# Kernel optimization log

Measured on AMD Instinct MI355X. Metric: run time of the kernel, lower is better.

## Reference

```python
import jax, jax.numpy as jnp
import numpy as np

N = 30000   # nodes
E = 240000  # edges
G = 16      # graphs in batch
DIMS = [1, 256, 512, 1024]
OUT = 1024

def _xavier(key, fan_in, fan_out):
    lim = float(np.sqrt(6.0 / (fan_in + fan_out)))
    return jax.random.uniform(key, (fan_in, fan_out), minval=-lim, maxval=lim, dtype=jnp.float32)

def setup_inputs() -> dict:
    key = jax.random.key(0)
    ks = jax.random.split(key, 8)
    x = jax.random.normal(ks[0], (N, DIMS[0]), dtype=jnp.float32)
    edge_index = jax.random.randint(ks[1], (2, E), 0, N, dtype=jnp.int64)
    batch = jnp.sort(jax.random.randint(ks[2], (N,), 0, G, dtype=jnp.int64))
    W1 = _xavier(ks[3], DIMS[0], DIMS[1]); b1 = jnp.zeros((DIMS[1],), jnp.float32)
    W2 = _xavier(ks[4], DIMS[1], DIMS[2]); b2 = jnp.zeros((DIMS[2],), jnp.float32)
    W3 = _xavier(ks[5], DIMS[2], DIMS[3]); b3 = jnp.zeros((DIMS[3],), jnp.float32)
    Wo = _xavier(ks[6], DIMS[3], OUT);     bo = jnp.zeros((OUT,), jnp.float32)
    return {"x": x, "edge_index": edge_index, "batch": batch,
            "W1": W1, "b1": b1, "W2": W2, "b2": b2, "W3": W3, "b3": b3,
            "Wo": Wo, "bo": bo}

def reference(x, edge_index, batch, W1, b1, W2, b2, W3, b3, Wo, bo):
    n = x.shape[0]
    loops = jnp.arange(n)
    # GCNConv adds self-loops, then symmetric deg^-1/2 normalization
    src = jnp.concatenate([edge_index[0], loops])
    dst = jnp.concatenate([edge_index[1], loops])
    deg = jnp.zeros((n,), jnp.float32).at[dst].add(1.0)  # >=1 due to self-loops
    dis = jax.lax.rsqrt(deg)
    norm = (dis[src] * dis[dst])[:, None]  # [E+N, 1]

    def gcn(h, W, b):
        h = h @ W                                   # linear (no bias in lin)
        agg = jnp.zeros_like(h).at[dst].add(h[src] * norm)  # scatter-add messages
        return agg + b                              # GCNConv bias

    h = jax.nn.relu(gcn(x, W1, b1))
    h = jax.nn.relu(gcn(h, W2, b2))
    h = jax.nn.relu(gcn(h, W3, b3))
    # global mean pool over graphs
    sums = jnp.zeros((G, h.shape[1]), h.dtype).at[batch].add(h)
    cnt = jnp.zeros((G,), h.dtype).at[batch].add(1.0)
    pooled = sums / jnp.maximum(cnt, 1.0)[:, None]
    return pooled @ Wo + bo
```

## Files before the change

### kernel.cpp

```cpp
#include <hip/hip_runtime.h>
#include <hip/hip_bf16.h>
#include <stdint.h>

#define N_NODES 30000
#define E_EDGES 240000
#define NGRAPH  16
#define D1      256
#define D2      512
#define D3      1024
#define DOUT    1024
#define M_PAD   30720
#define NT_M    240
#define CAP     40

typedef unsigned short ushort_t;
typedef short short8 __attribute__((ext_vector_type(8)));
typedef float f32x4 __attribute__((ext_vector_type(4)));

__device__ __forceinline__ float bf2f(ushort_t u) {
    union { unsigned int i; float f; } v; v.i = ((unsigned int)u) << 16; return v.f;
}
__device__ __forceinline__ ushort_t f2bf(float x) {
    union { float f; unsigned int i; } v; v.f = x;
    unsigned int r = v.i + 0x7fffu + ((v.i >> 16) & 1u);
    return (ushort_t)(r >> 16);
}

__device__ __forceinline__ void gl_lds16(const ushort_t* g, ushort_t* l) {
    __builtin_amdgcn_global_load_lds(
        (const __attribute__((address_space(1))) void*)(g),
        (__attribute__((address_space(3))) void*)(l), 16, 0, 0);
}

__global__ void k_detect(const void* w1, const void* ei, int* flags) {
    int lane = threadIdx.x & 63;
    const ushort_t* h = (const ushort_t*)w1;
    float v = fabsf(bf2f(h[lane * 2]));
    unsigned long long badf = __ballot(!(v <= 0.25f));
    const int* e = (const int*)ei;
    unsigned long long badi = __ballot(e[lane * 2 + 1] != 0);
    if (threadIdx.x == 0) {
        flags[0] = (badf == 0ull) ? 1 : 0;
        flags[1] = (badi == 0ull) ? 1 : 0;
    }
}

__global__ void k_setup(const void* x, const void* batch, const void* w1, const void* b1,
                        const void* b2, const void* b3, const void* bo,
                        const void* W2, const void* W3,
                        float* xf, int* batch32, float* W1f, float* b1f, float* b2f,
                        float* b3f, float* bof, ushort_t* Wt2, ushort_t* Wt3,
                        int* slotcnt, float* pooled, float* pooled2, const int* flags) {
    int isbf = flags[0];
    int bid = blockIdx.x;
    int tid = threadIdx.x;
    if (bid < 492) {
        int i = bid * 256 + tid;
        if (i < 3072) {
            const void* src; float* dst; int idx;
            if      (i < 256)  { src = w1; dst = W1f; idx = i; }
            else if (i < 512)  { src = b1; dst = b1f; idx = i - 256; }
            else if (i < 1024) { src = b2; dst = b2f; idx = i - 512; }
            else if (i < 2048) { src = b3; dst = b3f; idx = i - 1024; }
            else               { src = bo; dst = bof; idx = i - 2048; }
            dst[idx] = isbf ? bf2f(((const ushort_t*)src)[idx]) : ((const float*)src)[idx];
        } else if (i < 33072) {
            int idx = i - 3072;
            xf[idx] = isbf ? bf2f(((const ushort_t*)x)[idx]) : ((const float*)x)[idx];
        } else if (i < 63072) {
            int idx = i - 33072;
            batch32[idx] = flags[1] ? (int)((const long long*)batch)[idx]
                                    : ((const int*)batch)[idx];
        } else if (i < 93072) {
            slotcnt[i - 63072] = 0;
        } else if (i < 109456) {
            pooled[i - 93072] = 0.0f;
        } else if (i < 125840) {
            pooled2[i - 109456] = 0.0f;
        }
    } else {
        __shared__ ushort_t tile[32][33];
        int tb = bid - 492;
        const void* in; ushort_t* out; int R, C, bx, by;
        if (tb < 128) { in = W2; out = Wt2; R = D1; C = D2; bx = tb & 15; by = tb >> 4; }
        else { tb -= 128; in = W3; out = Wt3; R = D2; C = D3; bx = tb & 31; by = tb >> 5; }
        int tx = tid & 31, ty = tid >> 5;
        int c0 = bx * 32, r0 = by * 32;
        for (int i = ty; i < 32; i += 8) {
            size_t idx = (size_t)(r0 + i) * C + c0 + tx;
            tile[i][tx] = isbf ? ((const ushort_t*)in)[idx] : f2bf(((const float*)in)[idx]);
        }
        __syncthreads();
        for (int i = ty; i < 32; i += 8) out[(size_t)(c0 + i) * R + r0 + tx] = tile[tx][i];
    }
}

__global__ void k_edge_count(const void* ei, int* slotcnt, int* slots, const int* flags) {
    int e = blockIdx.x * 256 + threadIdx.x;
    if (e >= E_EDGES) return;
    int s, d;
    if (flags[1]) {
        s = (int)((const long long*)ei)[e];
        d = (int)((const long long*)ei)[E_EDGES + e];
    } else {
        s = ((const int*)ei)[e];
        d = ((const int*)ei)[E_EDGES + e];
    }
    if ((unsigned)s >= N_NODES || (unsigned)d >= N_NODES) return;
    int pos = atomicAdd(&slotcnt[d], 1);
    if (pos < CAP) slots[d * CAP + pos] = s;
}

__global__ void k_s1(const float* xf, const int* slotcnt, const int* slots,
                     const int* batch, float* dis, float* s1, float* cntg) {
    int b = blockIdx.x;
    if (b == 118) {
        int g = threadIdx.x;
        if (g >= NGRAPH) return;
        int lo0 = 0, hi0 = N_NODES;
        while (lo0 < hi0) { int m = (lo0 + hi0) >> 1; if (batch[m] < g) lo0 = m + 1; else hi0 = m; }
        int lo1 = lo0, hi1 = N_NODES;
        while (lo1 < hi1) { int m = (lo1 + hi1) >> 1; if (batch[m] < g + 1) lo1 = m + 1; else hi1 = m; }
        cntg[g] = (float)(lo1 - lo0);
        return;
    }
    int d = b * 256 + threadIdx.x;
    if (d >= N_NODES) return;
    int cd = slotcnt[d];
    float di = rsqrtf(1.0f + (float)cd);
    dis[d] = di;
    int cnt = cd < CAP ? cd : CAP;
    float acc = xf[d] * di;
    for (int k = 0; k < cnt; k++) {
        int s = slots[d * CAP + k];
        acc += xf[s] * rsqrtf(1.0f + (float)slotcnt[s]);
    }
    s1[d] = acc * di;
}

__global__ void k_agg1(const float* s1, const float* W1f, const float* b1f,
                       ushort_t* a2, const int* slots, const int* slotcnt, const float* dis) {
    int node = blockIdx.x * 4 + (threadIdx.x >> 6);
    int lane = threadIdx.x & 63;
    int c4 = lane * 4;
    float w[4], bb[4], a[4];
    #pragma unroll
    for (int j = 0; j < 4; j++) { w[j] = W1f[c4 + j]; bb[j] = b1f[c4 + j]; }
    float di = dis[node];
    int cnt = slotcnt[node]; cnt = cnt < CAP ? cnt : CAP;
    float sv = s1[node];
    float wsl = di * di;
    #pragma unroll
    for (int j = 0; j < 4; j++) a[j] = wsl * fmaxf(sv * w[j] + bb[j], 0.0f);
    for (int k = 0; k < cnt; k++) {
        int s = slots[node * CAP + k];
        float ss = s1[s];
        float wn = dis[s] * di;
        #pragma unroll
        for (int j = 0; j < 4; j++) a[j] += wn * fmaxf(ss * w[j] + bb[j], 0.0f);
    }
    uint2 o;
    o.x = (unsigned int)f2bf(a[0]) | ((unsigned int)f2bf(a[1]) << 16);
    o.y = (unsigned int)f2bf(a[2]) | ((unsigned int)f2bf(a[3]) << 16);
    *(uint2*)&a2[(size_t)node * D1 + c4] = o;
}

__global__ void k_agg2(const ushort_t* h, ushort_t* out, const int* slots,
                       const int* slotcnt, const float* dis) {
    int node = blockIdx.x * 4 + (threadIdx.x >> 6);
    int lane = threadIdx.x & 63;
    int c8 = lane * 8;
    float di = dis[node];
    int cnt = slotcnt[node]; cnt = cnt < CAP ? cnt : CAP;
    float w = di * di;
    const ushort_t* hp = h + c8;
    short8 p = *(const short8*)&hp[(size_t)node * D2];
    float a[8];
    #pragma unroll
    for (int j = 0; j < 8; j++) a[j] = w * bf2f((ushort_t)p[j]);
    if (cnt > 0) {
        int s0 = slots[node * CAP];
        short8 q0 = *(const short8*)&hp[(size_t)s0 * D2];
        float ws0 = dis[s0] * di;
        for (int k = 1; k < cnt; k++) {
            int s1i = slots[node * CAP + k];
            short8 q1 = *(const short8*)&hp[(size_t)s1i * D2];
            float ws1 = dis[s1i] * di;
            #pragma unroll
            for (int j = 0; j < 8; j++) a[j] += ws0 * bf2f((ushort_t)q0[j]);
            q0 = q1; ws0 = ws1;
        }
        #pragma unroll
        for (int j = 0; j < 8; j++) a[j] += ws0 * bf2f((ushort_t)q0[j]);
    }
    uint4 o;
    o.x = (unsigned int)f2bf(a[0]) | ((unsigned int)f2bf(a[1]) << 16);
    o.y = (unsigned int)f2bf(a[2]) | ((unsigned int)f2bf(a[3]) << 16);
    o.z = (unsigned int)f2bf(a[4]) | ((unsigned int)f2bf(a[5]) << 16);
    o.w = (unsigned int)f2bf(a[6]) | ((unsigned int)f2bf(a[7]) << 16);
    *(uint4*)&out[(size_t)node * D2 + c8] = o;
}

__global__ __launch_bounds__(256, 4) void k_gemm(const ushort_t* A, const ushort_t* Bt,
                                                 const float* bias, ushort_t* Cmat,
                                                 int K, int Ncols, int ntn) {
    __shared__ __align__(16) ushort_t As[2][128 * 32];
    __shared__ __align__(16) ushort_t Bs[2][128 * 32];
    int tid = threadIdx.x;
    int id = blockIdx.x;
    int xcd = id & 7, q = id >> 3;
    int rt = xcd * (NT_M / 8) + q / ntn;
    int ct = q % ntn;
    int bm0 = rt * 128, bn0 = ct * 128;
    int wave = tid >> 6, lane = tid & 63;
    int wm = (wave & 1) * 64, wn = (wave >> 1) * 64;
    int l15 = lane & 15, quad = lane >> 4;

    int m1 = tid >> 2, k1 = (tid & 3) << 3;
    int off1 = m1 * 32 + k1, off2 = off1 + 64 * 32;
    const ushort_t* pA1 = A + (size_t)(bm0 + m1) * K + k1;
    const ushort_t* pA2 = pA1 + (size_t)64 * K;
    const ushort_t* pB1 = Bt + (size_t)(bn0 + m1) * K + k1;
    const ushort_t* pB2 = pB1 + (size_t)64 * K;

    gl_lds16(pA1, &As[0][off1]); gl_lds16(pA2, &As[0][off2]);
    gl_lds16(pB1, &Bs[0][off1]); gl_lds16(pB2, &Bs[0][off2]);

    f32x4 acc[4][4];
    for (int a = 0; a < 4; a++)
        for (int b = 0; b < 4; b++)
            acc[a][b] = (f32x4){0.f, 0.f, 0.f, 0.f};

    int niter = K >> 5;
    for (int it = 0; it < niter; ++it) {
        __syncthreads();
        int cb = it & 1;
        int ktn = (it + 1) << 5;
        if (ktn < K) {
            int wb = cb ^ 1;
            gl_lds16(pA1 + ktn, &As[wb][off1]); gl_lds16(pA2 + ktn, &As[wb][off2]);
            gl_lds16(pB1 + ktn, &Bs[wb][off1]); gl_lds16(pB2 + ktn, &Bs[wb][off2]);
        }
        short8 af[4], bfr[4];
        for (int im = 0; im < 4; im++)
            af[im] = *(const short8*)&As[cb][(wm + im * 16 + l15) * 32 + quad * 8];
        for (int in = 0; in < 4; in++)
            bfr[in] = *(const short8*)&Bs[cb][(wn + in * 16 + l15) * 32 + quad * 8];
        for (int im = 0; im < 4; im++)
            for (int in = 0; in < 4; in++)
                acc[im][in] = __builtin_amdgcn_mfma_f32_16x16x32_bf16(af[im], bfr[in], acc[im][in], 0, 0, 0);
    }

    for (int im = 0; im < 4; im++) {
        int row = bm0 + wm + im * 16 + quad * 4;
        for (int in = 0; in < 4; in++) {
            int col = bn0 + wn + in * 16 + l15;
            float bv = bias[col];
            for (int r = 0; r < 4; r++) {
                float v = acc[im][in][r] + bv;
                v = v > 0.0f ? v : 0.0f;
                Cmat[(size_t)(row + r) * Ncols + col] = f2bf(v);
            }
        }
    }
}

__global__ __launch_bounds__(256, 4) void k_gemm_pool(const ushort_t* A, const ushort_t* Bt,
                                                      const float* bias, const int* batch,
                                                      float* pooled, int K, int ntn) {
    __shared__ __align__(16) ushort_t As[2][128 * 32];
    __shared__ __align__(16) ushort_t Bs[2][128 * 32];
    int tid = threadIdx.x;
    int id = blockIdx.x;
    int xcd = id & 7, q = id >> 3;
    int rt = xcd * (NT_M / 8) + q / ntn;
    int ct = q % ntn;
    int bm0 = rt * 128, bn0 = ct * 128;
    int wave = tid >> 6, lane = tid & 63;
    int wm = (wave & 1) * 64, wn = (wave >> 1) * 64;
    int l15 = lane & 15, quad = lane >> 4;

    int m1 = tid >> 2, k1 = (tid & 3) << 3;
    int off1 = m1 * 32 + k1, off2 = off1 + 64 * 32;
    const ushort_t* pA1 = A + (size_t)(bm0 + m1) * K + k1;
    const ushort_t* pA2 = pA1 + (size_t)64 * K;
    const ushort_t* pB1 = Bt + (size_t)(bn0 + m1) * K + k1;
    const ushort_t* pB2 = pB1 + (size_t)64 * K;

    gl_lds16(pA1, &As[0][off1]); gl_lds16(pA2, &As[0][off2]);
    gl_lds16(pB1, &Bs[0][off1]); gl_lds16(pB2, &Bs[0][off2]);

    f32x4 acc[4][4];
    for (int a = 0; a < 4; a++)
        for (int b = 0; b < 4; b++)
            acc[a][b] = (f32x4){0.f, 0.f, 0.f, 0.f};

    int niter = K >> 5;
    for (int it = 0; it < niter; ++it) {
        __syncthreads();
        int cb = it & 1;
        int ktn = (it + 1) << 5;
        if (ktn < K) {
            int wb = cb ^ 1;
            gl_lds16(pA1 + ktn, &As[wb][off1]); gl_lds16(pA2 + ktn, &As[wb][off2]);
            gl_lds16(pB1 + ktn, &Bs[wb][off1]); gl_lds16(pB2 + ktn, &Bs[wb][off2]);
        }
        short8 af[4], bfr[4];
        for (int im = 0; im < 4; im++)
            af[im] = *(const short8*)&As[cb][(wm + im * 16 + l15) * 32 + quad * 8];
        for (int in = 0; in < 4; in++)
            bfr[in] = *(const short8*)&Bs[cb][(wn + in * 16 + l15) * 32 + quad * 8];
        for (int im = 0; im < 4; im++)
            for (int in = 0; in < 4; in++)
                acc[im][in] = __builtin_amdgcn_mfma_f32_16x16x32_bf16(af[im], bfr[in], acc[im][in], 0, 0, 0);
    }

    __syncthreads();
    float* pl = (float*)&As[0][0];
    int* gtile = (int*)&Bs[0][0];
    for (int i = tid; i < NGRAPH * 128; i += 256) pl[i] = 0.0f;
    if (tid < 128) {
        int r = bm0 + tid; if (r > N_NODES - 1) r = N_NODES - 1;
        int g = batch[r]; g = g < 0 ? 0 : (g > NGRAPH - 1 ? NGRAPH - 1 : g);
        gtile[tid] = g;
    }
    __syncthreads();

    int gmin = gtile[0], gmax = gtile[127];
    if (gmin == gmax && bm0 + 127 < N_NODES) {
        float csum[4];
        #pragma unroll
        for (int in = 0; in < 4; in++) csum[in] = 0.0f;
        for (int im = 0; im < 4; im++) {
            #pragma unroll
            for (int in = 0; in < 4; in++) {
                float bv = bias[bn0 + wn + in * 16 + l15];
                #pragma unroll
                for (int r = 0; r < 4; r++)
                    csum[in] += fmaxf(acc[im][in][r] + bv, 0.0f);
            }
        }
        #pragma unroll
        for (int in = 0; in < 4; in++) {
            csum[in] += __shfl_xor(csum[in], 16);
            csum[in] += __shfl_xor(csum[in], 32);
        }
        if (quad == 0) {
            #pragma unroll
            for (int in = 0; in < 4; in++)
                atomicAdd(&pl[gmin * 128 + wn + in * 16 + l15], csum[in]);
        }
    } else {
        for (int im = 0; im < 4; im++) {
            int rl = wm + im * 16 + quad * 4;
            for (int in = 0; in < 4; in++) {
                int cl = wn + in * 16 + l15;
                float bv = bias[bn0 + cl];
                float vsum = 0.0f;
                int gprev = gtile[rl];
                for (int r = 0; r < 4; r++) {
                    int row = bm0 + rl + r;
                    float v = (row < N_NODES) ? fmaxf(acc[im][in][r] + bv, 0.0f) : 0.0f;
                    int g = gtile[rl + r];
                    if (g != gprev) {
                        atomicAdd(&pl[gprev * 128 + cl], vsum);
                        vsum = 0.0f; gprev = g;
                    }
                    vsum += v;
                }
                atomicAdd(&pl[gprev * 128 + cl], vsum);
            }
        }
    }
    __syncthreads();

    int span = (gmax - gmin + 1) * 128;
    for (int idx = tid; idx < span; idx += 256) {
        int g = gmin + (idx >> 7), cl = idx & 127;
        float v = pl[g * 128 + cl];
        if (v != 0.0f) atomicAdd(&pooled[g * DOUT + bn0 + cl], v);
    }
}

__global__ __launch_bounds__(256) void k_out_partial(const float* pooled, const void* Wo,
                                                     float* pooled2, const int* flags) {
    __shared__ float pl[NGRAPH * 32];
    int tid = threadIdx.x;
    int col = blockIdx.x * 256 + tid;
    int k0 = blockIdx.y * 32;
    for (int i = tid; i < NGRAPH * 32; i += 256) {
        int g = i >> 5, kk = i & 31;
        pl[i] = pooled[g * D3 + k0 + kk];
    }
    __syncthreads();
    int isbf = flags[0];
    float acc[NGRAPH];
    #pragma unroll
    for (int g = 0; g < NGRAPH; g++) acc[g] = 0.0f;
    #pragma unroll 4
    for (int kk = 0; kk < 32; kk++) {
        int k = k0 + kk;
        float wv = isbf ? bf2f(((const ushort_t*)Wo)[(size_t)k * DOUT + col])
                        : ((const float*)Wo)[(size_t)k * DOUT + col];
        #pragma unroll
        for (int g = 0; g < NGRAPH; g++)
            acc[g] += pl[g * 32 + kk] * wv;
    }
    #pragma unroll
    for (int g = 0; g < NGRAPH; g++)
        atomicAdd(&pooled2[g * DOUT + col], acc[g]);
}

__global__ void k_out_fin(const float* pooled2, const float* bof, const float* cntg,
                          void* out, const int* flags) {
    int i = blockIdx.x * 256 + threadIdx.x;
    int g = i >> 10, o = i & 1023;
    float c = cntg[g]; c = c > 1.0f ? c : 1.0f;
    float v = pooled2[i] / c + bof[o];
    if (flags[0]) ((ushort_t*)out)[i] = f2bf(v);
    else          ((float*)out)[i] = v;
}

extern "C" void kernel_launch(void* const* d_in, const int* in_sizes, int n_in,
                              void* d_out, int out_size, void* d_ws, size_t ws_size,
                              hipStream_t stream) {
    const void* x_raw  = d_in[0];
    const void* ei_raw = d_in[1];
    const void* b_raw  = d_in[2];
    const void* W1_raw = d_in[3];
    const void* b1_raw = d_in[4];
    const void* W2_raw = d_in[5];
    const void* b2_raw = d_in[6];
    const void* W3_raw = d_in[7];
    const void* b3_raw = d_in[8];
    const void* Wo_raw = d_in[9];
    const void* bo_raw = d_in[10];

    char* w = (char*)d_ws;
    size_t off = 0;
    auto alloc = [&](size_t b) { size_t o = off; off += (b + 255) & ~(size_t)255; return o; };
    int*   flags   = (int*)  (w + alloc(256));
    float* xf      = (float*)(w + alloc((size_t)N_NODES * 4));
    int*   batch32 = (int*)  (w + alloc((size_t)N_NODES * 4));
    float* W1f     = (float*)(w + alloc(D1 * 4));
    float* b1f     = (float*)(w + alloc(D1 * 4));
    float* b2f     = (float*)(w + alloc(D2 * 4));
    float* b3f     = (float*)(w + alloc(D3 * 4));
    float* bof     = (float*)(w + alloc(DOUT * 4));
    float* dis     = (float*)(w + alloc((size_t)N_NODES * 4));
    float* s1      = (float*)(w + alloc((size_t)N_NODES * 4));
    float* cntg    = (float*)(w + alloc(64));
    float* pooled  = (float*)(w + alloc((size_t)NGRAPH * DOUT * 4));
    float* pooled2 = (float*)(w + alloc((size_t)NGRAPH * DOUT * 4));
    int*   slotcnt = (int*)  (w + alloc((size_t)N_NODES * 4));
    int*   slots   = (int*)  (w + alloc((size_t)N_NODES * CAP * 4));
    ushort_t* Wt2  = (ushort_t*)(w + alloc((size_t)D2 * D1 * 2));
    ushort_t* Wt3  = (ushort_t*)(w + alloc((size_t)D3 * D2 * 2));
    ushort_t* slabA = (ushort_t*)(w + alloc((size_t)M_PAD * D2 * 2));
    ushort_t* a2 = slabA;
    ushort_t* a3 = slabA;
    ushort_t* h2   = (ushort_t*)(w + alloc((size_t)M_PAD * D2 * 2));

    int nb_e = (E_EDGES + 255) / 256;

    k_detect<<<1, 64, 0, stream>>>(W1_raw, ei_raw, flags);
    k_setup<<<1132, 256, 0, stream>>>(x_raw, b_raw, W1_raw, b1_raw, b2_raw, b3_raw, bo_raw,
                                      W2_raw, W3_raw, xf, batch32, W1f, b1f, b2f, b3f, bof,
                                      Wt2, Wt3, slotcnt, pooled, pooled2, flags);
    k_edge_count<<<nb_e, 256, 0, stream>>>(ei_raw, slotcnt, slots, flags);
    k_s1<<<119, 256, 0, stream>>>(xf, slotcnt, slots, batch32, dis, s1, cntg);

    k_agg1<<<N_NODES / 4, 256, 0, stream>>>(s1, W1f, b1f, a2, slots, slotcnt, dis);
    k_gemm<<<NT_M * (D2 / 128), 256, 0, stream>>>(a2, Wt2, b2f, h2, D1, D2, D2 / 128);
    k_agg2<<<N_NODES / 4, 256, 0, stream>>>(h2, a3, slots, slotcnt, dis);
    k_gemm_pool<<<NT_M * (D3 / 128), 256, 0, stream>>>(a3, Wt3, b3f, batch32, pooled, D2, D3 / 128);

    k_out_partial<<<dim3(DOUT / 256, D3 / 32), 256, 0, stream>>>(pooled, Wo_raw, pooled2, flags);
    k_out_fin<<<NGRAPH * DOUT / 256, 256, 0, stream>>>(pooled2, bof, cntg, d_out, flags);
}
```

Measured before the change: 249.9 us.

## Replace 128x128 GEMMs with 256x256-tile 8-wave pipelined MFMA kernel

```diff
diff --git a/kernel.cpp b/kernel.cpp
--- a/kernel.cpp
+++ b/kernel.cpp
@@ -10,7 +10,6 @@
 #define D3      1024
 #define DOUT    1024
 #define M_PAD   30720
-#define NT_M    240
 #define CAP     40
 
 typedef unsigned short ushort_t;
@@ -201,184 +200,195 @@
     *(uint4*)&out[(size_t)node * D2 + c8] = o;
 }
 
-__global__ __launch_bounds__(256, 4) void k_gemm(const ushort_t* A, const ushort_t* Bt,
-                                                 const float* bias, ushort_t* Cmat,
-                                                 int K, int Ncols, int ntn) {
-    __shared__ __align__(16) ushort_t As[2][128 * 32];
-    __shared__ __align__(16) ushort_t Bs[2][128 * 32];
-    int tid = threadIdx.x;
-    int id = blockIdx.x;
-    int xcd = id & 7, q = id >> 3;
-    int rt = xcd * (NT_M / 8) + q / ntn;
-    int ct = q % ntn;
-    int bm0 = rt * 128, bn0 = ct * 128;
-    int wave = tid >> 6, lane = tid & 63;
-    int wm = (wave & 1) * 64, wn = (wave >> 1) * 64;
-    int l15 = lane & 15, quad = lane >> 4;
-
-    int m1 = tid >> 2, k1 = (tid & 3) << 3;
-    int off1 = m1 * 32 + k1, off2 = off1 + 64 * 32;
-    const ushort_t* pA1 = A + (size_t)(bm0 + m1) * K + k1;
-    const ushort_t* pA2 = pA1 + (size_t)64 * K;
-    const ushort_t* pB1 = Bt + (size_t)(bn0 + m1) * K + k1;
-    const ushort_t* pB2 = pB1 + (size_t)64 * K;
-
-    gl_lds16(pA1, &As[0][off1]); gl_lds16(pA2, &As[0][off2]);
-    gl_lds16(pB1, &Bs[0][off1]); gl_lds16(pB2, &Bs[0][off2]);
-
-    f32x4 acc[4][4];
-    for (int a = 0; a < 4; a++)
+#define GPHASE(M0, M1, USTAGE, TAILWAIT)                                               \
+    a0 = rdA(slot, M0, inrow0); a1 = rdA(slot, M0, inrow1);                            \
+    a2r = rdA(slot, M1, inrow0); a3r = rdA(slot, M1, inrow1);                          \
+    if (hn) stage_unit(nslot, t + 1, USTAGE);                                          \
+    asm volatile("" ::: "memory");                                                     \
+    __builtin_amdgcn_s_barrier();                                                      \
+    asm volatile("s_waitcnt lgkmcnt(0)" ::: "memory");                                 \
+    __builtin_amdgcn_sched_barrier(0);                                                 \
+    __builtin_amdgcn_s_setprio(1);                                                     \
+    _Pragma("unroll")                                                                  \
+    for (int n = 0; n < 4; ++n) {                                                      \
+        acc[M0][n] = __builtin_amdgcn_mfma_f32_16x16x32_bf16(a0,  bf_[n][0], acc[M0][n], 0, 0, 0); \
+        acc[M0][n] = __builtin_amdgcn_mfma_f32_16x16x32_bf16(a1,  bf_[n][1], acc[M0][n], 0, 0, 0); \
+        acc[M1][n] = __builtin_amdgcn_mfma_f32_16x16x32_bf16(a2r, bf_[n][0], acc[M1][n], 0, 0, 0); \
+        acc[M1][n] = __builtin_amdgcn_mfma_f32_16x16x32_bf16(a3r, bf_[n][1], acc[M1][n], 0, 0, 0); \
+    }                                                                                  \
+    __builtin_amdgcn_s_setprio(0);                                                     \
+    TAILWAIT                                                                           \
+    asm volatile("" ::: "memory");                                                     \
+    __builtin_amdgcn_s_barrier();
+
+#define TW_NONE
+#define TW_P2 if (hn) { asm volatile("s_waitcnt vmcnt(4)" ::: "memory"); } \
+              else    { asm volatile("s_waitcnt vmcnt(0)" ::: "memory"); }
+#define TW_P4 if (hn) { asm volatile("s_waitcnt vmcnt(2)" ::: "memory"); } \
+              else    { asm volatile("s_waitcnt vmcnt(0)" ::: "memory"); }
+
+template<int POOL>
+__global__ __launch_bounds__(512, 2) void k_gemm8(const ushort_t* A, const ushort_t* Bt,
+                                                  const float* bias, const int* batch,
+                                                  float* pooled, ushort_t* Cmat,
+                                                  int K, int Ncols, int ntn, int NT) {
+    __shared__ __align__(16) ushort_t As[2][256 * 64];
+    __shared__ __align__(16) ushort_t Bs[2][256 * 64];
+    const int tid = threadIdx.x;
+    const int id = blockIdx.x;
+    const int xcd = id & 7, q = id >> 3;
+    const int rt = xcd * ((M_PAD / 256) / 8) + q / ntn;
+    const int ct = q % ntn;
+    const int bm0 = rt * 256, bn0 = ct * 256;
+    const int wave = tid >> 6, lane = tid & 63;
+    const int wr = wave >> 2, wc = wave & 3;
+    const int l15 = lane & 15, quad = lane >> 4;
+
+    const ushort_t* gA = A + (size_t)bm0 * K;
+    const ushort_t* gB = Bt + (size_t)bn0 * K;
+
+    auto stage_blk = [&](ushort_t* ldsbase, const ushort_t* gbase, int kt, int b) {
+        int row = b >> 3;
+        int kb = (b & 7) ^ (row & 7);
+        gl_lds16(gbase + (size_t)row * K + (kt << 6) + (kb << 3), ldsbase + (b << 3));
+    };
+    auto stage_unit = [&](int slot, int kt, int u) {
+        if (u == 0)      { stage_blk(Bs[slot], gB, kt, tid);        stage_blk(Bs[slot], gB, kt, tid + 512); }
+        else if (u == 1) { stage_blk(Bs[slot], gB, kt, tid + 1024); stage_blk(Bs[slot], gB, kt, tid + 1536); }
+        else if (u == 2) { stage_blk(As[slot], gA, kt, tid);        stage_blk(As[slot], gA, kt, tid + 1024); }
+        else             { stage_blk(As[slot], gA, kt, tid + 512);  stage_blk(As[slot], gA, kt, tid + 1536); }
+    };
+
+    const int swzx = (l15 & 7) << 4;
+    const int inrow0 = (quad * 16) ^ swzx;
+    const int inrow1 = (quad * 16 + 64) ^ swzx;
+    const int arowb = (wr * 128 + l15) * 128;
+    const int browb = (wc * 64 + l15) * 128;
+
+    auto rdA = [&](int slot, int m, int inr) -> short8 {
+        return *(const short8*)((const char*)As[slot] + arowb + m * 2048 + inr);
+    };
+    auto rdB = [&](int slot, int n, int inr) -> short8 {
+        return *(const short8*)((const char*)Bs[slot] + browb + n * 2048 + inr);
+    };
+
+    stage_unit(0, 0, 0); stage_unit(0, 0, 1); stage_unit(0, 0, 2); stage_unit(0, 0, 3);
+    asm volatile("s_waitcnt vmcnt(2)" ::: "memory");
+    __builtin_amdgcn_s_barrier();
+
+    f32x4 acc[8][4];
+    #pragma unroll
+    for (int a = 0; a < 8; a++)
+        #pragma unroll
         for (int b = 0; b < 4; b++)
             acc[a][b] = (f32x4){0.f, 0.f, 0.f, 0.f};
 
-    int niter = K >> 5;
-    for (int it = 0; it < niter; ++it) {
+    short8 bf_[4][2];
+    for (int t = 0; t < NT; ++t) {
+        const int slot = t & 1, nslot = slot ^ 1;
+        const bool hn = (t + 1) < NT;
+        short8 a0, a1, a2r, a3r;
+        #pragma unroll
+        for (int n = 0; n < 4; ++n) {
+            bf_[n][0] = rdB(slot, n, inrow0);
+            bf_[n][1] = rdB(slot, n, inrow1);
+        }
+        GPHASE(0, 1, 0, TW_NONE)
+        GPHASE(2, 3, 1, TW_P2)
+        GPHASE(4, 5, 2, TW_NONE)
+        GPHASE(6, 7, 3, TW_P4)
+    }
+
+    if (POOL == 0) {
+        #pragma unroll
+        for (int im = 0; im < 8; im++) {
+            int row = bm0 + wr * 128 + im * 16 + quad * 4;
+            #pragma unroll
+            for (int in = 0; in < 4; in++) {
+                int col = bn0 + wc * 64 + in * 16 + l15;
+                float bv = bias[col];
+                #pragma unroll
+                for (int r = 0; r < 4; r++) {
+                    float v = acc[im][in][r] + bv;
+                    v = v > 0.0f ? v : 0.0f;
+                    Cmat[(size_t)(row + r) * Ncols + col] = f2bf(v);
+                }
+            }
+        }
+    } else {
+        asm volatile("s_waitcnt vmcnt(0) lgkmcnt(0)" ::: "memory");
         __syncthreads();
-        int cb = it & 1;
-        int ktn = (it + 1) << 5;
-        if (ktn < K) {
-            int wb = cb ^ 1;
-            gl_lds16(pA1 + ktn, &As[wb][off1]); gl_lds16(pA2 + ktn, &As[wb][off2]);
-            gl_lds16(pB1 + ktn, &Bs[wb][off1]); gl_lds16(pB2 + ktn, &Bs[wb][off2]);
-        }
-        short8 af[4], bfr[4];
-        for (int im = 0; im < 4; im++)
-            af[im] = *(const short8*)&As[cb][(wm + im * 16 + l15) * 32 + quad * 8];
-        for (int in = 0; in < 4; in++)
-            bfr[in] = *(const short8*)&Bs[cb][(wn + in * 16 + l15) * 32 + quad * 8];
-        for (int im = 0; im < 4; im++)
-            for (int in = 0; in < 4; in++)
-                acc[im][in] = __builtin_amdgcn_mfma_f32_16x16x32_bf16(af[im], bfr[in], acc[im][in], 0, 0, 0);
-    }
-
-    for (int im = 0; im < 4; im++) {
-        int row = bm0 + wm + im * 16 + quad * 4;
-        for (int in = 0; in < 4; in++) {
-            int col = bn0 + wn + in * 16 + l15;
-            float bv = bias[col];
-            for (int r = 0; r < 4; r++) {
-                float v = acc[im][in][r] + bv;
-                v = v > 0.0f ? v : 0.0f;
-                Cmat[(size_t)(row + r) * Ncols + col] = f2bf(v);
-            }
-        }
-    }
-}
-
-__global__ __launch_bounds__(256, 4) void k_gemm_pool(const ushort_t* A, const ushort_t* Bt,
-                                                      const float* bias, const int* batch,
-                                                      float* pooled, int K, int ntn) {
-    __shared__ __align__(16) ushort_t As[2][128 * 32];
-    __shared__ __align__(16) ushort_t Bs[2][128 * 32];
-    int tid = threadIdx.x;
-    int id = blockIdx.x;
-    int xcd = id & 7, q = id >> 3;
-    int rt = xcd * (NT_M / 8) + q / ntn;
-    int ct = q % ntn;
-    int bm0 = rt * 128, bn0 = ct * 128;
-    int wave = tid >> 6, lane = tid & 63;
-    int wm = (wave & 1) * 64, wn = (wave >> 1) * 64;
-    int l15 = lane & 15, quad = lane >> 4;
-
-    int m1 = tid >> 2, k1 = (tid & 3) << 3;
-    int off1 = m1 * 32 + k1, off2 = off1 + 64 * 32;
-    const ushort_t* pA1 = A + (size_t)(bm0 + m1) * K + k1;
-    const ushort_t* pA2 = pA1 + (size_t)64 * K;
-    const ushort_t* pB1 = Bt + (size_t)(bn0 + m1) * K + k1;
-    const ushort_t* pB2 = pB1 + (size_t)64 * K;
-
-    gl_lds16(pA1, &As[0][off1]); gl_lds16(pA2, &As[0][off2]);
-    gl_lds16(pB1, &Bs[0][off1]); gl_lds16(pB2, &Bs[0][off2]);
-
-    f32x4 acc[4][4];
-    for (int a = 0; a < 4; a++)
-        for (int b = 0; b < 4; b++)
-            acc[a][b] = (f32x4){0.f, 0.f, 0.f, 0.f};
-
-    int niter = K >> 5;
-    for (int it = 0; it < niter; ++it) {
+        float* pl = (float*)&As[0][0];
+        int* gtile = (int*)&Bs[0][0];
+        for (int i = tid; i < NGRAPH * 256; i += 512) pl[i] = 0.0f;
+        if (tid < 256) {
+            int r = bm0 + tid; if (r > N_NODES - 1) r = N_NODES - 1;
+            int g = batch[r]; g = g < 0 ? 0 : (g > NGRAPH - 1 ? NGRAPH - 1 : g);
+            gtile[tid] = g;
+        }
         __syncthreads();
-        int cb = it & 1;
-        int ktn = (it + 1) << 5;
-        if (ktn < K) {
-            int wb = cb ^ 1;
-            gl_lds16(pA1 + ktn, &As[wb][off1]); gl_lds16(pA2 + ktn, &As[wb][off2]);
-            gl_lds16(pB1 + ktn, &Bs[wb][off1]); gl_lds16(pB2 + ktn, &Bs[wb][off2]);
-        }
-        short8 af[4], bfr[4];
-        for (int im = 0; im < 4; im++)
-            af[im] = *(const short8*)&As[cb][(wm + im * 16 + l15) * 32 + quad * 8];
-        for (int in = 0; in < 4; in++)
-            bfr[in] = *(const short8*)&Bs[cb][(wn + in * 16 + l15) * 32 + quad * 8];
-        for (int im = 0; im < 4; im++)
-            for (int in = 0; in < 4; in++)
-                acc[im][in] = __builtin_amdgcn_mfma_f32_16x16x32_bf16(af[im], bfr[in], acc[im][in], 0, 0, 0);
-    }
-
-    __syncthreads();
-    float* pl = (float*)&As[0][0];
-    int* gtile = (int*)&Bs[0][0];
-    for (int i = tid; i < NGRAPH * 128; i += 256) pl[i] = 0.0f;
-    if (tid < 128) {
-        int r = bm0 + tid; if (r > N_NODES - 1) r = N_NODES - 1;
-        int g = batch[r]; g = g < 0 ? 0 : (g > NGRAPH - 1 ? NGRAPH - 1 : g);
-        gtile[tid] = g;
-    }
-    __syncthreads();
-
-    int gmin = gtile[0], gmax = gtile[127];
-    if (gmin == gmax && bm0 + 127 < N_NODES) {
-        float csum[4];
-        #pragma unroll
-        for (int in = 0; in < 4; in++) csum[in] = 0.0f;
-        for (int im = 0; im < 4; im++) {
+
+        int gmin = gtile[0], gmax = gtile[255];
+        if (gmin == gmax && bm0 + 255 < N_NODES) {
+            float csum[4];
+            float bv[4];
             #pragma unroll
             for (int in = 0; in < 4; in++) {
-                float bv = bias[bn0 + wn + in * 16 + l15];
+                csum[in] = 0.0f;
+                bv[in] = bias[bn0 + wc * 64 + in * 16 + l15];
+            }
+            #pragma unroll
+            for (int im = 0; im < 8; im++) {
                 #pragma unroll
-                for (int r = 0; r < 4; r++)
-                    csum[in] += fmaxf(acc[im][in][r] + bv, 0.0f);
-            }
-        }
-        #pragma unroll
-        for (int in = 0; in < 4; in++) {
-            csum[in] += __shfl_xor(csum[in], 16);
-            csum[in] += __shfl_xor(csum[in], 32);
-        }
-        if (quad == 0) {
-            #pragma unroll
-            for (int in = 0; in < 4; in++)
-                atomicAdd(&pl[gmin * 128 + wn + in * 16 + l15], csum[in]);
-        }
-    } else {
-        for (int im = 0; im < 4; im++) {
-            int rl = wm + im * 16 + quad * 4;
+                for (int in = 0; in < 4; in++) {
+                    #pragma unroll
+                    for (int r = 0; r < 4; r++)
+                        csum[in] += fmaxf(acc[im][in][r] + bv[in], 0.0f);
+                }
+            }
+            #pragma unroll
             for (int in = 0; in < 4; in++) {
-                int cl = wn + in * 16 + l15;
-                float bv = bias[bn0 + cl];
-                float vsum = 0.0f;
-                int gprev = gtile[rl];
-                for (int r = 0; r < 4; r++) {
-                    int row = bm0 + rl + r;
-                    float v = (row < N_NODES) ? fmaxf(acc[im][in][r] + bv, 0.0f) : 0.0f;
-                    int g = gtile[rl + r];
-                    if (g != gprev) {
-                        atomicAdd(&pl[gprev * 128 + cl], vsum);
-                        vsum = 0.0f; gprev = g;
+                csum[in] += __shfl_xor(csum[in], 16);
+                csum[in] += __shfl_xor(csum[in], 32);
+            }
+            if (quad == 0) {
+                #pragma unroll
+                for (int in = 0; in < 4; in++)
+                    atomicAdd(&pl[gmin * 256 + wc * 64 + in * 16 + l15], csum[in]);
+            }
+        } else {
+            #pragma unroll
+            for (int im = 0; im < 8; im++) {
+                int rl = wr * 128 + im * 16 + quad * 4;
+                #pragma unroll
+                for (int in = 0; in < 4; in++) {
+                    int cl = wc * 64 + in * 16 + l15;
+                    float bv = bias[bn0 + cl];
+                    float vsum = 0.0f;
+                    int gprev = gtile[rl];
+                    #pragma unroll
+                    for (int r = 0; r < 4; r++) {
+                        int row = bm0 + rl + r;
+                        float v = (row < N_NODES) ? fmaxf(acc[im][in][r] + bv, 0.0f) : 0.0f;
+                        int g = gtile[rl + r];
+                        if (g != gprev) {
+                            atomicAdd(&pl[gprev * 256 + cl], vsum);
+                            vsum = 0.0f; gprev = g;
+                        }
+                        vsum += v;
                     }
-                    vsum += v;
+                    atomicAdd(&pl[gprev * 256 + cl], vsum);
                 }
-                atomicAdd(&pl[gprev * 128 + cl], vsum);
-            }
-        }
-    }
-    __syncthreads();
-
-    int span = (gmax - gmin + 1) * 128;
-    for (int idx = tid; idx < span; idx += 256) {
-        int g = gmin + (idx >> 7), cl = idx & 127;
-        float v = pl[g * 128 + cl];
-        if (v != 0.0f) atomicAdd(&pooled[g * DOUT + bn0 + cl], v);
+            }
+        }
+        __syncthreads();
+
+        int span = (gmax - gmin + 1) * 256;
+        for (int idx = tid; idx < span; idx += 512) {
+            int g = gmin + (idx >> 8), cl = idx & 255;
+            float v = pl[g * 256 + cl];
+            if (v != 0.0f) atomicAdd(&pooled[g * DOUT + bn0 + cl], v);
+        }
     }
 }
 
@@ -471,9 +481,13 @@
     k_s1<<<119, 256, 0, stream>>>(xf, slotcnt, slots, batch32, dis, s1, cntg);
 
     k_agg1<<<N_NODES / 4, 256, 0, stream>>>(s1, W1f, b1f, a2, slots, slotcnt, dis);
-    k_gemm<<<NT_M * (D2 / 128), 256, 0, stream>>>(a2, Wt2, b2f, h2, D1, D2, D2 / 128);
+    k_gemm8<0><<<(M_PAD / 256) * (D2 / 256), 512, 0, stream>>>(a2, Wt2, b2f, nullptr,
+                                                               nullptr, h2, D1, D2,
+                                                               D2 / 256, D1 / 64);
     k_agg2<<<N_NODES / 4, 256, 0, stream>>>(h2, a3, slots, slotcnt, dis);
-    k_gemm_pool<<<NT_M * (D3 / 128), 256, 0, stream>>>(a3, Wt3, b3f, batch32, pooled, D2, D3 / 128);
+    k_gemm8<1><<<(M_PAD / 256) * (D3 / 256), 512, 0, stream>>>(a3, Wt3, b3f, batch32,
+                                                               pooled, nullptr, D2, D3,
+                                                               D3 / 256, D2 / 64);
 
     k_out_partial<<<dim3(DOUT / 256, D3 / 32), 256, 0, stream>>>(pooled, Wo_raw, pooled2, flags);
     k_out_fin<<<NGRAPH * DOUT / 256, 256, 0, stream>>>(pooled2, bof, cntg, d_out, flags);
```

Result: slower. 270.8 us (+8.4%).
